# Performance work log

Measured on AMD Instinct MI355X. Metric: run time of the kernel, lower is better.

Reference implementation:

```python
import jax, jax.numpy as jnp
import numpy as np

D_MODEL = 1024
H = 16
D_H = D_MODEL // H
B = 8
S = 1024
NEG_INF = -1e9


def setup_inputs() -> dict:
    key = jax.random.key(0)
    ks = jax.random.split(key, 8)
    Qs = jax.random.normal(ks[0], (B, S, D_MODEL), dtype=jnp.float32)
    Ks = jax.random.normal(ks[1], (B, S, D_MODEL), dtype=jnp.float32)
    Vs = jax.random.normal(ks[2], (B, S, D_MODEL), dtype=jnp.float32)
    mask_3d = jnp.zeros((B, S, S), dtype=bool)
    # Parameters: torch.rand -> uniform[0,1) for per-head projections
    W_Q = jax.random.uniform(ks[3], (H, D_MODEL, D_H), dtype=jnp.float32)
    W_K = jax.random.uniform(ks[4], (H, D_MODEL, D_H), dtype=jnp.float32)
    W_V = jax.random.uniform(ks[5], (H, D_MODEL, D_H), dtype=jnp.float32)
    # Output nn.Linear(h*d_h, d_model): weight [d_model, h*d_h], bias [d_model]
    lim = 1.0 / np.sqrt(H * D_H)
    W_out = jax.random.uniform(ks[6], (D_MODEL, H * D_H), minval=-lim, maxval=lim, dtype=jnp.float32)
    b_out = jax.random.uniform(ks[7], (D_MODEL,), minval=-lim, maxval=lim, dtype=jnp.float32)
    return {"Qs": Qs, "Ks": Ks, "Vs": Vs, "mask_3d": mask_3d,
            "W_Q": W_Q, "W_K": W_K, "W_V": W_V, "W_out": W_out, "b_out": b_out}


def reference(Qs, Ks, Vs, mask_3d, W_Q, W_K, W_V, W_out, b_out):
    # Fused per-head projections: avoid the explicit repeat in the torch code.
    q = jnp.einsum('bsk,hkl->bhsl', Qs, W_Q)  # [B,H,S,D_H]
    k = jnp.einsum('bsk,hkl->bhsl', Ks, W_K)
    v = jnp.einsum('bsk,hkl->bhsl', Vs, W_V)
    scale = 1.0 / jnp.sqrt(jnp.asarray(D_H, dtype=q.dtype))
    scores = jnp.einsum('bhqd,bhkd->bhqk', q, k) * scale  # [B,H,S,S]
    scores = jnp.where(mask_3d[:, None, :, :], NEG_INF, scores)
    attn = jax.nn.softmax(scores, axis=-1)
    out = jnp.einsum('bhqk,bhkd->bhqd', attn, v)  # [B,H,S,D_H]
    # chunk along head-batch dim then cat along feature dim == head-major concat
    out = jnp.transpose(out, (0, 2, 1, 3)).reshape(B, S, H * D_H)
    return out @ W_out.T + b_out
```

## Files before the change

kernel.cpp:

```cpp
#include <hip/hip_runtime.h>

#define DM 1024
#define H_ 16
#define DH 64
#define B_ 8
#define S_ 1024

typedef _Float16 half8 __attribute__((ext_vector_type(8)));
typedef _Float16 half4 __attribute__((ext_vector_type(4)));
typedef float f32x4 __attribute__((ext_vector_type(4)));
typedef float f32x16 __attribute__((ext_vector_type(16)));
typedef unsigned int uint;

static __device__ inline uint pkh(float a, float b) {
    _Float16 ha = (_Float16)a, hb = (_Float16)b;
    unsigned short ua = __builtin_bit_cast(unsigned short, ha);
    unsigned short ub = __builtin_bit_cast(unsigned short, hb);
    return (uint)ua | ((uint)ub << 16);
}
#define PSWAP(d, s) asm volatile("v_permlane32_swap_b32 %0, %1" : "+v"(d), "+v"(s))

static __device__ __forceinline__ void gload16(const _Float16* g, _Float16* l) {
    __builtin_amdgcn_global_load_lds(
        (const __attribute__((address_space(1))) unsigned int*)(const void*)g,
        (__attribute__((address_space(3))) unsigned int*)(void*)l,
        16, 0, 0);
}

__global__ __launch_bounds__(256) void packw_k(
    const float* __restrict__ WQ, const float* __restrict__ WK,
    const float* __restrict__ WV,
    _Float16* __restrict__ wqh, _Float16* __restrict__ wql,
    _Float16* __restrict__ wkh, _Float16* __restrict__ wkl,
    _Float16* __restrict__ wv)
{
    __shared__ __align__(16) _Float16 Lh[64][72];
    __shared__ __align__(16) _Float16 Ll[64][72];
    const int t = threadIdx.x;
    const int kb = blockIdx.x;
    const int h  = blockIdx.y;

    #pragma unroll
    for (int s = 0; s < 3; ++s) {
        const float* W = (s == 0) ? WQ : ((s == 1) ? WK : WV);
        const int krow = t >> 2, lc = t & 3;
        const float* rp = W + (((size_t)h * 1024 + kb * 64 + krow) * 64 + lc * 16);
        #pragma unroll
        for (int q4 = 0; q4 < 4; ++q4) {
            float4 f = ((const float4*)rp)[q4];
            float vv0 = f.x, vv1 = f.y, vv2 = f.z, vv3 = f.w;
            int l0 = lc * 16 + q4 * 4;
            _Float16 h0 = (_Float16)vv0; Lh[l0 + 0][krow] = h0; Ll[l0 + 0][krow] = (_Float16)(vv0 - (float)h0);
            _Float16 h1 = (_Float16)vv1; Lh[l0 + 1][krow] = h1; Ll[l0 + 1][krow] = (_Float16)(vv1 - (float)h1);
            _Float16 h2 = (_Float16)vv2; Lh[l0 + 2][krow] = h2; Ll[l0 + 2][krow] = (_Float16)(vv2 - (float)h2);
            _Float16 h3 = (_Float16)vv3; Lh[l0 + 3][krow] = h3; Ll[l0 + 3][krow] = (_Float16)(vv3 - (float)h3);
        }
        __syncthreads();
        const int l = t >> 2, pc = t & 3;
        #pragma unroll
        for (int hp = 0; hp < 2; ++hp) {
            int p = pc + 4 * hp;
            int lc2 = p ^ (l & 7);
            half8 vh = *(const half8*)&Lh[l][lc2 * 8];
            half8 vl = *(const half8*)&Ll[l][lc2 * 8];
            size_t off = (size_t)(h * 64 + l) * DM + kb * 64 + p * 8;
            if (s == 0) { *(half8*)(wqh + off) = vh; *(half8*)(wql + off) = vl; }
            else if (s == 1) { *(half8*)(wkh + off) = vh; *(half8*)(wkl + off) = vl; }
            else { *(half8*)(wv + off) = vh; }
        }
        __syncthreads();
    }
}

__global__ __launch_bounds__(256) void packo_k(
    const float* __restrict__ WO, _Float16* __restrict__ wo)
{
    int idx8 = blockIdx.x * 256 + threadIdx.x;
    int n = idx8 >> 7;
    int c = idx8 & 127;
    int p = (c & ~7) | ((c & 7) ^ (n & 7));
    const float* rp = WO + ((size_t)n * DM + c * 8);
    float4 a = ((const float4*)rp)[0];
    float4 b = ((const float4*)rp)[1];
    half8 v;
    v[0] = (_Float16)a.x; v[1] = (_Float16)a.y; v[2] = (_Float16)a.z; v[3] = (_Float16)a.w;
    v[4] = (_Float16)b.x; v[5] = (_Float16)b.y; v[6] = (_Float16)b.z; v[7] = (_Float16)b.w;
    *(half8*)(wo + (size_t)n * DM + p * 8) = v;
}

__global__ __launch_bounds__(256) void scan_k(
    const unsigned char* __restrict__ mask, unsigned char* __restrict__ scan)
{
    __shared__ int s_red[4];
    const int t = threadIdx.x;
    const int q64 = blockIdx.x, k64 = blockIdx.y, b = blockIdx.z;
    uint4 mv = *(const uint4*)(mask + ((size_t)b * S_ + q64 * 64 + (t >> 2)) * S_ + k64 * 64 + (t & 3) * 16);
    int a = (mv.x | mv.y | mv.z | mv.w) != 0;
    unsigned long long bal = __ballot(a);
    if ((t & 63) == 0) s_red[t >> 6] = (bal != 0ull);
    __syncthreads();
    if (t == 0)
        scan[(b * 16 + q64) * 16 + k64] =
            (unsigned char)(s_red[0] | s_red[1] | s_red[2] | s_red[3]);
}

__global__ __launch_bounds__(256) void gemm_split_k(
    const float* __restrict__ A0, const float* __restrict__ A1,
    const _Float16* __restrict__ Bh0, const _Float16* __restrict__ Bl0,
    const _Float16* __restrict__ Bh1, const _Float16* __restrict__ Bl1,
    _Float16* __restrict__ Chi0, _Float16* __restrict__ Clo0,
    _Float16* __restrict__ Chi1, _Float16* __restrict__ Clo1)
{
    const int lid = blockIdx.x + 8 * blockIdx.y + 512 * blockIdx.z;
    const int xcd = lid & 7, k2 = lid >> 3;
    const int G = xcd * 16 + (k2 >> 3);
    const int bxv = k2 & 7, byv = G & 63, z = G >> 6;

    const float* A = z ? A1 : A0;
    const _Float16* Bh = z ? Bh1 : Bh0;
    const _Float16* Bl = z ? Bl1 : Bl0;
    _Float16* Chi = z ? Chi1 : Chi0;
    _Float16* Clo = z ? Clo1 : Clo0;

    __shared__ __align__(16) _Float16 SM[34816];
    _Float16* Ah  = SM;
    _Float16* Al  = SM + 9216;
    _Float16* Bhs = SM + 18432;
    _Float16* Bls = SM + 26624;

    const int t = threadIdx.x;
    const int lane = t & 63;
    const int w = t >> 6;
    const int wm = (w >> 1) * 64;
    const int wn = (w & 1) * 64;
    const int l15 = lane & 15;
    const int l4g = lane >> 4;

    const int bm = byv * 128;
    const int bn = bxv * 128;

    f32x4 acc[4][4] = {};

    const int arow = t >> 4, ac4 = t & 15;
    float4 ar[8];
    auto aload = [&](int KT) {
        #pragma unroll
        for (int i = 0; i < 8; ++i)
            ar[i] = *(const float4*)(A + (size_t)(bm + arow + 16 * i) * DM + KT * 64 + ac4 * 4);
    };
    auto awr = [&]() {
        #pragma unroll
        for (int i = 0; i < 8; ++i) {
            float4 v = ar[i];
            half4 hv, lv;
            hv[0] = (_Float16)v.x; lv[0] = (_Float16)(v.x - (float)hv[0]);
            hv[1] = (_Float16)v.y; lv[1] = (_Float16)(v.y - (float)hv[1]);
            hv[2] = (_Float16)v.z; lv[2] = (_Float16)(v.z - (float)hv[2]);
            hv[3] = (_Float16)v.w; lv[3] = (_Float16)(v.w - (float)hv[3]);
            *(half4*)&Ah[(arow + 16 * i) * 72 + ac4 * 4] = hv;
            *(half4*)&Al[(arow + 16 * i) * 72 + ac4 * 4] = lv;
        }
    };
    auto bgl = [&](int KT) {
        #pragma unroll
        for (int j = 0; j < 4; ++j) {
            int rr = w * 32 + j * 8 + (lane >> 3);
            const size_t so = (size_t)(bn + rr) * DM + KT * 64 + (lane & 7) * 8;
            gload16(Bh + so, &Bhs[(w * 32 + j * 8) * 64]);
            gload16(Bl + so, &Bls[(w * 32 + j * 8) * 64]);
        }
    };

    aload(0);
    bgl(0);
    for (int kt = 0; kt < 16; ++kt) {
        awr();
        __syncthreads();
        if (kt < 15) aload(kt + 1);
        #pragma unroll
        for (int ks = 0; ks < 2; ++ks) {
            half8 ah[4], al[4], bh[4], bl[4];
            #pragma unroll
            for (int mi = 0; mi < 4; ++mi) {
                ah[mi] = *(const half8*)&Ah[(wm + mi * 16 + l15) * 72 + ks * 32 + l4g * 8];
                al[mi] = *(const half8*)&Al[(wm + mi * 16 + l15) * 72 + ks * 32 + l4g * 8];
            }
            #pragma unroll
            for (int ni = 0; ni < 4; ++ni) {
                int row = wn + ni * 16 + l15;
                int slot = (ks * 4 + l4g) ^ (l15 & 7);
                bh[ni] = *(const half8*)&Bhs[row * 64 + slot * 8];
                bl[ni] = *(const half8*)&Bls[row * 64 + slot * 8];
            }
            #pragma unroll
            for (int mi = 0; mi < 4; ++mi)
                #pragma unroll
                for (int ni = 0; ni < 4; ++ni) {
                    acc[mi][ni] = __builtin_amdgcn_mfma_f32_16x16x32_f16(ah[mi], bh[ni], acc[mi][ni], 0, 0, 0);
                    acc[mi][ni] = __builtin_amdgcn_mfma_f32_16x16x32_f16(ah[mi], bl[ni], acc[mi][ni], 0, 0, 0);
                    acc[mi][ni] = __builtin_amdgcn_mfma_f32_16x16x32_f16(al[mi], bh[ni], acc[mi][ni], 0, 0, 0);
                }
        }
        __syncthreads();
        if (kt < 15) bgl(kt + 1);
    }

    #pragma unroll
    for (int mi = 0; mi < 4; ++mi)
        #pragma unroll
        for (int ni = 0; ni < 4; ++ni) {
            int col = bn + wn + ni * 16 + l15;
            #pragma unroll
            for (int r = 0; r < 4; ++r) {
                int row = bm + wm + mi * 16 + l4g * 4 + r;
                float val = acc[mi][ni][r];
                _Float16 hv = (_Float16)val;
                Chi[(size_t)row * DM + col] = hv;
                Clo[(size_t)row * DM + col] = (_Float16)(val - (float)hv);
            }
        }
}

__global__ __launch_bounds__(256) void gemm_v_k(
    const float* __restrict__ A, const _Float16* __restrict__ Bt,
    _Float16* __restrict__ C)
{
    const int lid = blockIdx.x + 8 * blockIdx.y;
    const int xcd = lid & 7, k2 = lid >> 3;
    const int G = xcd * 8 + (k2 >> 3);
    const int bxv = k2 & 7, byv = G;

    __shared__ __align__(16) _Float16 SM[25600];
    _Float16* As  = SM;
    _Float16* Bsb = SM + 9216;

    const int t = threadIdx.x;
    const int lane = t & 63;
    const int w = t >> 6;
    const int wm = (w >> 1) * 64;
    const int wn = (w & 1) * 64;
    const int l15 = lane & 15;
    const int l4g = lane >> 4;

    const int bm = byv * 128;
    const int bn = bxv * 128;

    f32x4 acc[4][4] = {};

    const int arow = t >> 4, ac4 = t & 15;
    float4 ar[8];
    auto aload = [&](int KT) {
        #pragma unroll
        for (int i = 0; i < 8; ++i)
            ar[i] = *(const float4*)(A + (size_t)(bm + arow + 16 * i) * DM + KT * 64 + ac4 * 4);
    };
    auto awr = [&]() {
        #pragma unroll
        for (int i = 0; i < 8; ++i) {
            float4 v = ar[i];
            half4 hv;
            hv[0] = (_Float16)v.x; hv[1] = (_Float16)v.y;
            hv[2] = (_Float16)v.z; hv[3] = (_Float16)v.w;
            *(half4*)&As[(arow + 16 * i) * 72 + ac4 * 4] = hv;
        }
    };
    auto bgl = [&](int KT, int buf) {
        _Float16* Bd = Bsb + buf * 8192;
        #pragma unroll
        for (int j = 0; j < 4; ++j) {
            int rr = w * 32 + j * 8 + (lane >> 3);
            gload16(Bt + (size_t)(bn + rr) * DM + KT * 64 + (lane & 7) * 8,
                    &Bd[(w * 32 + j * 8) * 64]);
        }
    };

    aload(0);
    bgl(0, 0);
    for (int kt = 0; kt < 16; ++kt) {
        const _Float16* Bcur = Bsb + (kt & 1) * 8192;
        awr();
        __syncthreads();
        if (kt < 15) { aload(kt + 1); bgl(kt + 1, (kt + 1) & 1); }
        #pragma unroll
        for (int ks = 0; ks < 2; ++ks) {
            half8 a[4], b[4];
            #pragma unroll
            for (int mi = 0; mi < 4; ++mi)
                a[mi] = *(const half8*)&As[(wm + mi * 16 + l15) * 72 + ks * 32 + l4g * 8];
            #pragma unroll
            for (int ni = 0; ni < 4; ++ni) {
                int row = wn + ni * 16 + l15;
                int slot = (ks * 4 + l4g) ^ (l15 & 7);
                b[ni] = *(const half8*)&Bcur[row * 64 + slot * 8];
            }
            #pragma unroll
            for (int mi = 0; mi < 4; ++mi)
                #pragma unroll
                for (int ni = 0; ni < 4; ++ni)
                    acc[mi][ni] = __builtin_amdgcn_mfma_f32_16x16x32_f16(a[mi], b[ni], acc[mi][ni], 0, 0, 0);
        }
        __syncthreads();
    }

    _Float16* Tw = SM + w * 4608;
    #pragma unroll
    for (int mi = 0; mi < 4; ++mi)
        #pragma unroll
        for (int ni = 0; ni < 4; ++ni)
            #pragma unroll
            for (int r = 0; r < 4; ++r)
                Tw[(ni * 16 + l15) * 72 + mi * 16 + l4g * 4 + r] = (_Float16)acc[mi][ni][r];
    __syncthreads();
    {
        const int mg0 = bm + wm;
        const int b = mg0 >> 10, s0 = mg0 & 1023;
        _Float16* op = C + ((size_t)b * DM + (bn + wn + lane)) * S_ + s0;
        #pragma unroll
        for (int c8 = 0; c8 < 8; ++c8)
            *(half8*)(op + c8 * 8) = *(const half8*)&Tw[lane * 72 + c8 * 8];
    }
}

__global__ __launch_bounds__(256) void gemm_out_k(
    const _Float16* __restrict__ A, const _Float16* __restrict__ Bt,
    float* __restrict__ C, const float* __restrict__ bias)
{
    const int lid = blockIdx.x + 8 * blockIdx.y;
    const int xcd = lid & 7, k2 = lid >> 3;
    const int G = xcd * 8 + (k2 >> 3);
    const int bxv = k2 & 7, byv = G;

    __shared__ __align__(16) _Float16 SM[25600];
    _Float16* As  = SM;
    _Float16* Bsb = SM + 9216;

    const int t = threadIdx.x;
    const int lane = t & 63;
    const int w = t >> 6;
    const int wm = (w >> 1) * 64;
    const int wn = (w & 1) * 64;
    const int l15 = lane & 15;
    const int l4g = lane >> 4;

    const int bm = byv * 128;
    const int bn = bxv * 128;

    f32x4 acc[4][4] = {};

    uint4 arr[4];
    auto aload = [&](int KT) {
        #pragma unroll
        for (int i = 0; i < 4; ++i)
            arr[i] = *(const uint4*)(A + (size_t)(bm + (t >> 3) + 32 * i) * DM + KT * 64 + (t & 7) * 8);
    };
    auto awr = [&]() {
        #pragma unroll
        for (int i = 0; i < 4; ++i)
            *(uint4*)&As[((t >> 3) + 32 * i) * 72 + (t & 7) * 8] = arr[i];
    };
    auto bgl = [&](int KT, int buf) {
        _Float16* Bd = Bsb + buf * 8192;
        #pragma unroll
        for (int j = 0; j < 4; ++j) {
            int rr = w * 32 + j * 8 + (lane >> 3);
            gload16(Bt + (size_t)(bn + rr) * DM + KT * 64 + (lane & 7) * 8,
                    &Bd[(w * 32 + j * 8) * 64]);
        }
    };

    aload(0);
    bgl(0, 0);
    for (int kt = 0; kt < 16; ++kt) {
        const _Float16* Bcur = Bsb + (kt & 1) * 8192;
        awr();
        __syncthreads();
        if (kt < 15) { aload(kt + 1); bgl(kt + 1, (kt + 1) & 1); }
        #pragma unroll
        for (int ks = 0; ks < 2; ++ks) {
            half8 a[4], b[4];
            #pragma unroll
            for (int mi = 0; mi < 4; ++mi)
                a[mi] = *(const half8*)&As[(wm + mi * 16 + l15) * 72 + ks * 32 + l4g * 8];
            #pragma unroll
            for (int ni = 0; ni < 4; ++ni) {
                int row = wn + ni * 16 + l15;
                int slot = (ks * 4 + l4g) ^ (l15 & 7);
                b[ni] = *(const half8*)&Bcur[row * 64 + slot * 8];
            }
            #pragma unroll
            for (int mi = 0; mi < 4; ++mi)
                #pragma unroll
                for (int ni = 0; ni < 4; ++ni)
                    acc[mi][ni] = __builtin_amdgcn_mfma_f32_16x16x32_f16(a[mi], b[ni], acc[mi][ni], 0, 0, 0);
        }
        __syncthreads();
    }

    #pragma unroll
    for (int mi = 0; mi < 4; ++mi)
        #pragma unroll
        for (int ni = 0; ni < 4; ++ni) {
            int col = bn + wn + ni * 16 + l15;
            #pragma unroll
            for (int r = 0; r < 4; ++r) {
                int row = bm + wm + mi * 16 + l4g * 4 + r;
                C[(size_t)row * DM + col] = acc[mi][ni][r] + bias[col];
            }
        }
}

__global__ __launch_bounds__(256) void attn_k(
    const _Float16* __restrict__ qhg, const _Float16* __restrict__ qlg,
    const _Float16* __restrict__ khg, const _Float16* __restrict__ klg,
    const _Float16* __restrict__ vtg, const unsigned char* __restrict__ maskg,
    const unsigned char* __restrict__ scanp, _Float16* __restrict__ ho)
{
    __shared__ __align__(16) _Float16 Kh[64][72];
    __shared__ __align__(16) _Float16 Kl[64][72];
    __shared__ __align__(16) _Float16 Vt[64][72];

    const int t = threadIdx.x;
    const int lane = t & 63;
    const int w = t >> 6;
    const int l31 = lane & 31;
    const int hi = lane >> 5;

    const int j = blockIdx.y + 16 * blockIdx.z;
    const int head = 16 * blockIdx.x + (j >> 3);
    const int qt = j & 7;
    const int h = head & 15;
    const int b = head >> 4;

    const int colbase = h * DH;
    const int qrow = qt * 128 + w * 32 + l31;

    half8 qfh[4], qfl[4];
    {
        const size_t base = ((size_t)b * S_ + qrow) * DM + colbase;
        #pragma unroll
        for (int ds = 0; ds < 4; ++ds) {
            qfh[ds] = *(const half8*)(qhg + base + ds * 16 + hi * 8);
            qfl[ds] = *(const half8*)(qlg + base + ds * 16 + hi * 8);
        }
    }

    float m_q = -1e30f, ls = 0.0f;
    f32x16 accO0 = {};
    f32x16 accO1 = {};

    const int r0 = t >> 3;
    const int c0 = (t & 7) * 8;
    const _Float16* kph = khg + ((size_t)b * S_) * DM + colbase;
    const _Float16* kpl = klg + ((size_t)b * S_) * DM + colbase;
    const _Float16* vp  = vtg + ((size_t)b * DM + colbase) * S_;
    const unsigned char* sc0 = scanp + (b * 16 + 2 * qt) * 16;
    const unsigned char* sc1 = scanp + (b * 16 + 2 * qt + 1) * 16;

    uint4 akh0, akh1, akl0, akl1, av0, av1;
#define ALOAD(KT) do { \
        akh0 = *(const uint4*)(kph + (size_t)((KT) * 64 + r0) * DM + c0);       \
        akh1 = *(const uint4*)(kph + (size_t)((KT) * 64 + 32 + r0) * DM + c0);  \
        akl0 = *(const uint4*)(kpl + (size_t)((KT) * 64 + r0) * DM + c0);       \
        akl1 = *(const uint4*)(kpl + (size_t)((KT) * 64 + 32 + r0) * DM + c0);  \
        av0  = *(const uint4*)(vp + (size_t)r0 * S_ + (KT) * 64 + c0);          \
        av1  = *(const uint4*)(vp + (size_t)(32 + r0) * S_ + (KT) * 64 + c0);   \
    } while (0)
#define AWRITE() do { \
        *(uint4*)&Kh[r0][c0] = akh0; *(uint4*)&Kh[32 + r0][c0] = akh1; \
        *(uint4*)&Kl[r0][c0] = akl0; *(uint4*)&Kl[32 + r0][c0] = akl1; \
        *(uint4*)&Vt[r0][c0] = av0;  *(uint4*)&Vt[32 + r0][c0] = av1;  \
    } while (0)

    ALOAD(0);
    AWRITE();
    int msk = sc0[0] | sc1[0];

    const float SC = 0.125f * 1.44269504089f;

    for (int kt = 0; kt < 16; ++kt) {
        __syncthreads();
        const int mskcur = msk;
        if (kt < 15) {
            ALOAD(kt + 1);
            msk = sc0[kt + 1] | sc1[kt + 1];
        }

        f32x16 sa0 = {}, sa1 = {};
        #pragma unroll
        for (int ds = 0; ds < 4; ++ds) {
            half8 kh0 = *(const half8*)&Kh[l31][ds * 16 + hi * 8];
            half8 kl0 = *(const half8*)&Kl[l31][ds * 16 + hi * 8];
            half8 kh1 = *(const half8*)&Kh[32 + l31][ds * 16 + hi * 8];
            half8 kl1 = *(const half8*)&Kl[32 + l31][ds * 16 + hi * 8];
            sa0 = __builtin_amdgcn_mfma_f32_32x32x16_f16(kh0, qfh[ds], sa0, 0, 0, 0);
            sa0 = __builtin_amdgcn_mfma_f32_32x32x16_f16(kh0, qfl[ds], sa0, 0, 0, 0);
            sa0 = __builtin_amdgcn_mfma_f32_32x32x16_f16(kl0, qfh[ds], sa0, 0, 0, 0);
            sa1 = __builtin_amdgcn_mfma_f32_32x32x16_f16(kh1, qfh[ds], sa1, 0, 0, 0);
            sa1 = __builtin_amdgcn_mfma_f32_32x32x16_f16(kh1, qfl[ds], sa1, 0, 0, 0);
            sa1 = __builtin_amdgcn_mfma_f32_32x32x16_f16(kl1, qfh[ds], sa1, 0, 0, 0);
        }
        #pragma unroll
        for (int e = 0; e < 16; ++e) { sa0[e] *= SC; sa1[e] *= SC; }

        if (mskcur) {
            const unsigned char* mrow = maskg + ((size_t)b * S_ + qrow) * S_ + kt * 64;
            #pragma unroll
            for (int e = 0; e < 16; ++e) {
                int kl_ = (e & 3) + 8 * (e >> 2) + 4 * hi;
                if (mrow[kl_]) sa0[e] = -1e9f;
                if (mrow[32 + kl_]) sa1[e] = -1e9f;
            }
        }

        float rm = sa0[0];
        #pragma unroll
        for (int e = 1; e < 16; ++e) rm = fmaxf(rm, sa0[e]);
        #pragma unroll
        for (int e = 0; e < 16; ++e) rm = fmaxf(rm, sa1[e]);
        rm = fmaxf(rm, __shfl_xor(rm, 32));
        const float mn = fmaxf(m_q, rm);
        const float sfac = exp2f(m_q - mn);
        m_q = mn;
        float rs = 0.0f;
        #pragma unroll
        for (int e = 0; e < 16; ++e) { sa0[e] = exp2f(sa0[e] - mn); rs += sa0[e]; }
        #pragma unroll
        for (int e = 0; e < 16; ++e) { sa1[e] = exp2f(sa1[e] - mn); rs += sa1[e]; }
        rs += __shfl_xor(rs, 32);
        ls = ls * sfac + rs;
        #pragma unroll
        for (int e = 0; e < 16; ++e) { accO0[e] *= sfac; accO1[e] *= sfac; }

        half8 pf[4];
        {
            uint c0_ = pkh(sa0[0], sa0[1]),  c1_ = pkh(sa0[2], sa0[3]);
            uint c2_ = pkh(sa0[4], sa0[5]),  c3_ = pkh(sa0[6], sa0[7]);
            uint c4_ = pkh(sa0[8], sa0[9]),  c5_ = pkh(sa0[10], sa0[11]);
            uint c6_ = pkh(sa0[12], sa0[13]), c7_ = pkh(sa0[14], sa0[15]);
            PSWAP(c0_, c2_); PSWAP(c1_, c3_);
            PSWAP(c4_, c6_); PSWAP(c5_, c7_);
            uint4 u0 = {c0_, c1_, c2_, c3_}, u1 = {c4_, c5_, c6_, c7_};
            pf[0] = __builtin_bit_cast(half8, u0);
            pf[1] = __builtin_bit_cast(half8, u1);
        }
        {
            uint c0_ = pkh(sa1[0], sa1[1]),  c1_ = pkh(sa1[2], sa1[3]);
            uint c2_ = pkh(sa1[4], sa1[5]),  c3_ = pkh(sa1[6], sa1[7]);
            uint c4_ = pkh(sa1[8], sa1[9]),  c5_ = pkh(sa1[10], sa1[11]);
            uint c6_ = pkh(sa1[12], sa1[13]), c7_ = pkh(sa1[14], sa1[15]);
            PSWAP(c0_, c2_); PSWAP(c1_, c3_);
            PSWAP(c4_, c6_); PSWAP(c5_, c7_);
            uint4 u0 = {c0_, c1_, c2_, c3_}, u1 = {c4_, c5_, c6_, c7_};
            pf[2] = __builtin_bit_cast(half8, u0);
            pf[3] = __builtin_bit_cast(half8, u1);
        }
        #pragma unroll
        for (int kc = 0; kc < 4; ++kc) {
            half8 vf0 = *(const half8*)&Vt[l31][kc * 16 + hi * 8];
            half8 vf1 = *(const half8*)&Vt[32 + l31][kc * 16 + hi * 8];
            accO0 = __builtin_amdgcn_mfma_f32_32x32x16_f16(vf0, pf[kc], accO0, 0, 0, 0);
            accO1 = __builtin_amdgcn_mfma_f32_32x32x16_f16(vf1, pf[kc], accO1, 0, 0, 0);
        }

        __syncthreads();
        if (kt < 15) AWRITE();
    }
#undef ALOAD
#undef AWRITE

    const float inv = 1.0f / ls;
    _Float16* orow = ho + ((size_t)b * S_ + qrow) * DM + colbase;
    #pragma unroll
    for (int g2 = 0; g2 < 4; ++g2) {
        half4 hv0, hv1;
        #pragma unroll
        for (int e = 0; e < 4; ++e) {
            hv0[e] = (_Float16)(accO0[g2 * 4 + e] * inv);
            hv1[e] = (_Float16)(accO1[g2 * 4 + e] * inv);
        }
        *(half4*)(orow + g2 * 8 + hi * 4) = hv0;
        *(half4*)(orow + 32 + g2 * 8 + hi * 4) = hv1;
    }
}

extern "C" void kernel_launch(void* const* d_in, const int* in_sizes, int n_in,
                              void* d_out, int out_size, void* d_ws, size_t ws_size,
                              hipStream_t stream)
{
    const float* Qs = (const float*)d_in[0];
    const float* Ks = (const float*)d_in[1];
    const float* Vs = (const float*)d_in[2];
    const unsigned char* mask = (const unsigned char*)d_in[3];
    const float* WQ = (const float*)d_in[4];
    const float* WK = (const float*)d_in[5];
    const float* WV = (const float*)d_in[6];
    const float* WO = (const float*)d_in[7];
    const float* bo = (const float*)d_in[8];

    char* ws = (char*)d_ws;
    const size_t MB = 1024 * 1024;
    _Float16* wqh = (_Float16*)(ws + 0 * MB);
    _Float16* wql = (_Float16*)(ws + 2 * MB);
    _Float16* wkh = (_Float16*)(ws + 4 * MB);
    _Float16* wkl = (_Float16*)(ws + 6 * MB);
    _Float16* wv  = (_Float16*)(ws + 8 * MB);
    _Float16* wo  = (_Float16*)(ws + 10 * MB);
    _Float16* qhi = (_Float16*)(ws + 12 * MB);
    _Float16* qlo = (_Float16*)(ws + 28 * MB);
    _Float16* khi = (_Float16*)(ws + 44 * MB);
    _Float16* klo = (_Float16*)(ws + 60 * MB);
    _Float16* vt  = (_Float16*)(ws + 76 * MB);
    _Float16* hh  = (_Float16*)(ws + 92 * MB);
    unsigned char* scan = (unsigned char*)(ws + 108 * MB);

    packw_k<<<dim3(16, 16), 256, 0, stream>>>(WQ, WK, WV, wqh, wql, wkh, wkl, wv);
    packo_k<<<512, 256, 0, stream>>>(WO, wo);
    scan_k<<<dim3(16, 16, 8), 256, 0, stream>>>(mask, scan);

    gemm_split_k<<<dim3(8, 64, 2), 256, 0, stream>>>(
        Qs, Ks, wqh, wql, wkh, wkl, qhi, qlo, khi, klo);

    gemm_v_k<<<dim3(8, 64), 256, 0, stream>>>(Vs, wv, vt);

    attn_k<<<dim3(8, 16, 8), 256, 0, stream>>>(qhi, qlo, khi, klo, vt, mask, scan, hh);

    gemm_out_k<<<dim3(8, 64), 256, 0, stream>>>(hh, wo, (float*)d_out, bo);
}
```

Before: 310.1 us.

## Use 512-thread split GEMM, lazy softmax rescale, pkrtz packing and MFMA priority

The split-precision Q/K projection GEMM moves to 512 threads per block with 32-row warp tiles and an XOR-swizzled unpadded A tile in LDS, halving per-thread accumulators and loads. In the attention kernel the per-element score scaling is folded into an FMA inside exp2, and the running max and output rescale are only updated when some lane's row max exceeds the old max by a threshold. Probability packing switches to the hardware round-toward-zero pack instruction, and MFMA blocks are wrapped in s_setprio raises. These target register pressure, LDS padding and VALU work in the softmax, at the cost of slightly different rounding and a threshold-based lazy rescale that allows exp values to grow before renormalising.

```diff
diff --git a/kernel.cpp b/kernel.cpp
--- a/kernel.cpp
+++ b/kernel.cpp
@@ -8,15 +8,14 @@
 
 typedef _Float16 half8 __attribute__((ext_vector_type(8)));
 typedef _Float16 half4 __attribute__((ext_vector_type(4)));
+typedef __fp16 fp16x2 __attribute__((ext_vector_type(2)));
 typedef float f32x4 __attribute__((ext_vector_type(4)));
 typedef float f32x16 __attribute__((ext_vector_type(16)));
 typedef unsigned int uint;
 
-static __device__ inline uint pkh(float a, float b) {
-    _Float16 ha = (_Float16)a, hb = (_Float16)b;
-    unsigned short ua = __builtin_bit_cast(unsigned short, ha);
-    unsigned short ub = __builtin_bit_cast(unsigned short, hb);
-    return (uint)ua | ((uint)ub << 16);
+static __device__ __forceinline__ uint pkrtz(float a, float b) {
+    fp16x2 h = __builtin_amdgcn_cvt_pkrtz(a, b);
+    return __builtin_bit_cast(uint, h);
 }
 #define PSWAP(d, s) asm volatile("v_permlane32_swap_b32 %0, %1" : "+v"(d), "+v"(s))
 
@@ -104,7 +103,7 @@
             (unsigned char)(s_red[0] | s_red[1] | s_red[2] | s_red[3]);
 }
 
-__global__ __launch_bounds__(256) void gemm_split_k(
+__global__ __launch_bounds__(512) void gemm_split_k(
     const float* __restrict__ A0, const float* __restrict__ A1,
     const _Float16* __restrict__ Bh0, const _Float16* __restrict__ Bl0,
     const _Float16* __restrict__ Bh1, const _Float16* __restrict__ Bl1,
@@ -122,16 +121,16 @@
     _Float16* Chi = z ? Chi1 : Chi0;
     _Float16* Clo = z ? Clo1 : Clo0;
 
-    __shared__ __align__(16) _Float16 SM[34816];
+    __shared__ __align__(16) _Float16 SM[32768];
     _Float16* Ah  = SM;
-    _Float16* Al  = SM + 9216;
-    _Float16* Bhs = SM + 18432;
-    _Float16* Bls = SM + 26624;
+    _Float16* Al  = SM + 8192;
+    _Float16* Bhs = SM + 16384;
+    _Float16* Bls = SM + 24576;
 
     const int t = threadIdx.x;
     const int lane = t & 63;
     const int w = t >> 6;
-    const int wm = (w >> 1) * 64;
+    const int wm = (w >> 1) * 32;
     const int wn = (w & 1) * 64;
     const int l15 = lane & 15;
     const int l4g = lane >> 4;
@@ -139,35 +138,37 @@
     const int bm = byv * 128;
     const int bn = bxv * 128;
 
-    f32x4 acc[4][4] = {};
-
-    const int arow = t >> 4, ac4 = t & 15;
-    float4 ar[8];
+    f32x4 acc[2][4] = {};
+
+    float4 ar[4];
     auto aload = [&](int KT) {
         #pragma unroll
-        for (int i = 0; i < 8; ++i)
-            ar[i] = *(const float4*)(A + (size_t)(bm + arow + 16 * i) * DM + KT * 64 + ac4 * 4);
+        for (int i = 0; i < 4; ++i)
+            ar[i] = *(const float4*)(A + (size_t)(bm + (t >> 4) + 32 * i) * DM + KT * 64 + (t & 15) * 4);
     };
     auto awr = [&]() {
         #pragma unroll
-        for (int i = 0; i < 8; ++i) {
+        for (int i = 0; i < 4; ++i) {
+            int row = (t >> 4) + 32 * i;
+            int c4 = t & 15;
             float4 v = ar[i];
             half4 hv, lv;
             hv[0] = (_Float16)v.x; lv[0] = (_Float16)(v.x - (float)hv[0]);
             hv[1] = (_Float16)v.y; lv[1] = (_Float16)(v.y - (float)hv[1]);
             hv[2] = (_Float16)v.z; lv[2] = (_Float16)(v.z - (float)hv[2]);
             hv[3] = (_Float16)v.w; lv[3] = (_Float16)(v.w - (float)hv[3]);
-            *(half4*)&Ah[(arow + 16 * i) * 72 + ac4 * 4] = hv;
-            *(half4*)&Al[(arow + 16 * i) * 72 + ac4 * 4] = lv;
+            int off = row * 64 + (((c4 >> 1) ^ (row & 7)) * 8) + (c4 & 1) * 4;
+            *(half4*)&Ah[off] = hv;
+            *(half4*)&Al[off] = lv;
         }
     };
     auto bgl = [&](int KT) {
         #pragma unroll
-        for (int j = 0; j < 4; ++j) {
-            int rr = w * 32 + j * 8 + (lane >> 3);
+        for (int j = 0; j < 2; ++j) {
+            int rr = w * 16 + j * 8 + (lane >> 3);
             const size_t so = (size_t)(bn + rr) * DM + KT * 64 + (lane & 7) * 8;
-            gload16(Bh + so, &Bhs[(w * 32 + j * 8) * 64]);
-            gload16(Bl + so, &Bls[(w * 32 + j * 8) * 64]);
+            gload16(Bh + so, &Bhs[(w * 16 + j * 8) * 64]);
+            gload16(Bl + so, &Bls[(w * 16 + j * 8) * 64]);
         }
     };
 
@@ -179,21 +180,24 @@
         if (kt < 15) aload(kt + 1);
         #pragma unroll
         for (int ks = 0; ks < 2; ++ks) {
-            half8 ah[4], al[4], bh[4], bl[4];
-            #pragma unroll
-            for (int mi = 0; mi < 4; ++mi) {
-                ah[mi] = *(const half8*)&Ah[(wm + mi * 16 + l15) * 72 + ks * 32 + l4g * 8];
-                al[mi] = *(const half8*)&Al[(wm + mi * 16 + l15) * 72 + ks * 32 + l4g * 8];
+            half8 ah[2], al[2], bh[4], bl[4];
+            const int slotx = (ks * 4 + l4g);
+            #pragma unroll
+            for (int mi = 0; mi < 2; ++mi) {
+                int r = wm + mi * 16 + l15;
+                int off = r * 64 + (slotx ^ (l15 & 7)) * 8;
+                ah[mi] = *(const half8*)&Ah[off];
+                al[mi] = *(const half8*)&Al[off];
             }
             #pragma unroll
             for (int ni = 0; ni < 4; ++ni) {
-                int row = wn + ni * 16 + l15;
-                int slot = (ks * 4 + l4g) ^ (l15 & 7);
-                bh[ni] = *(const half8*)&Bhs[row * 64 + slot * 8];
-                bl[ni] = *(const half8*)&Bls[row * 64 + slot * 8];
+                int r = wn + ni * 16 + l15;
+                int off = r * 64 + (slotx ^ (l15 & 7)) * 8;
+                bh[ni] = *(const half8*)&Bhs[off];
+                bl[ni] = *(const half8*)&Bls[off];
             }
             #pragma unroll
-            for (int mi = 0; mi < 4; ++mi)
+            for (int mi = 0; mi < 2; ++mi)
                 #pragma unroll
                 for (int ni = 0; ni < 4; ++ni) {
                     acc[mi][ni] = __builtin_amdgcn_mfma_f32_16x16x32_f16(ah[mi], bh[ni], acc[mi][ni], 0, 0, 0);
@@ -206,7 +210,7 @@
     }
 
     #pragma unroll
-    for (int mi = 0; mi < 4; ++mi)
+    for (int mi = 0; mi < 2; ++mi)
         #pragma unroll
         for (int ni = 0; ni < 4; ++ni) {
             int col = bn + wn + ni * 16 + l15;
@@ -476,6 +480,7 @@
     int msk = sc0[0] | sc1[0];
 
     const float SC = 0.125f * 1.44269504089f;
+    const float THRRAW = 8.0f / SC;
 
     for (int kt = 0; kt < 16; ++kt) {
         __syncthreads();
@@ -486,6 +491,7 @@
         }
 
         f32x16 sa0 = {}, sa1 = {};
+        __builtin_amdgcn_s_setprio(1);
         #pragma unroll
         for (int ds = 0; ds < 4; ++ds) {
             half8 kh0 = *(const half8*)&Kh[l31][ds * 16 + hi * 8];
@@ -499,8 +505,7 @@
             sa1 = __builtin_amdgcn_mfma_f32_32x32x16_f16(kh1, qfl[ds], sa1, 0, 0, 0);
             sa1 = __builtin_amdgcn_mfma_f32_32x32x16_f16(kl1, qfh[ds], sa1, 0, 0, 0);
         }
-        #pragma unroll
-        for (int e = 0; e < 16; ++e) { sa0[e] *= SC; sa1[e] *= SC; }
+        __builtin_amdgcn_s_setprio(0);
 
         if (mskcur) {
             const unsigned char* mrow = maskg + ((size_t)b * S_ + qrow) * S_ + kt * 64;
@@ -518,25 +523,29 @@
         #pragma unroll
         for (int e = 0; e < 16; ++e) rm = fmaxf(rm, sa1[e]);
         rm = fmaxf(rm, __shfl_xor(rm, 32));
-        const float mn = fmaxf(m_q, rm);
-        const float sfac = exp2f(m_q - mn);
-        m_q = mn;
+        if (__any(rm > m_q + THRRAW)) {
+            const float mn = fmaxf(m_q, rm);
+            const float sfac = exp2f((m_q - mn) * SC);
+            m_q = mn;
+            ls *= sfac;
+            #pragma unroll
+            for (int e = 0; e < 16; ++e) { accO0[e] *= sfac; accO1[e] *= sfac; }
+        }
+        const float nmn = -m_q * SC;
         float rs = 0.0f;
         #pragma unroll
-        for (int e = 0; e < 16; ++e) { sa0[e] = exp2f(sa0[e] - mn); rs += sa0[e]; }
-        #pragma unroll
-        for (int e = 0; e < 16; ++e) { sa1[e] = exp2f(sa1[e] - mn); rs += sa1[e]; }
+        for (int e = 0; e < 16; ++e) { sa0[e] = exp2f(fmaf(sa0[e], SC, nmn)); rs += sa0[e]; }
+        #pragma unroll
+        for (int e = 0; e < 16; ++e) { sa1[e] = exp2f(fmaf(sa1[e], SC, nmn)); rs += sa1[e]; }
         rs += __shfl_xor(rs, 32);
-        ls = ls * sfac + rs;
-        #pragma unroll
-        for (int e = 0; e < 16; ++e) { accO0[e] *= sfac; accO1[e] *= sfac; }
+        ls += rs;
 
         half8 pf[4];
         {
-            uint c0_ = pkh(sa0[0], sa0[1]),  c1_ = pkh(sa0[2], sa0[3]);
-            uint c2_ = pkh(sa0[4], sa0[5]),  c3_ = pkh(sa0[6], sa0[7]);
-            uint c4_ = pkh(sa0[8], sa0[9]),  c5_ = pkh(sa0[10], sa0[11]);
-            uint c6_ = pkh(sa0[12], sa0[13]), c7_ = pkh(sa0[14], sa0[15]);
+            uint c0_ = pkrtz(sa0[0], sa0[1]),  c1_ = pkrtz(sa0[2], sa0[3]);
+            uint c2_ = pkrtz(sa0[4], sa0[5]),  c3_ = pkrtz(sa0[6], sa0[7]);
+            uint c4_ = pkrtz(sa0[8], sa0[9]),  c5_ = pkrtz(sa0[10], sa0[11]);
+            uint c6_ = pkrtz(sa0[12], sa0[13]), c7_ = pkrtz(sa0[14], sa0[15]);
             PSWAP(c0_, c2_); PSWAP(c1_, c3_);
             PSWAP(c4_, c6_); PSWAP(c5_, c7_);
             uint4 u0 = {c0_, c1_, c2_, c3_}, u1 = {c4_, c5_, c6_, c7_};
@@ -544,16 +553,17 @@
             pf[1] = __builtin_bit_cast(half8, u1);
         }
         {
-            uint c0_ = pkh(sa1[0], sa1[1]),  c1_ = pkh(sa1[2], sa1[3]);
-            uint c2_ = pkh(sa1[4], sa1[5]),  c3_ = pkh(sa1[6], sa1[7]);
-            uint c4_ = pkh(sa1[8], sa1[9]),  c5_ = pkh(sa1[10], sa1[11]);
-            uint c6_ = pkh(sa1[12], sa1[13]), c7_ = pkh(sa1[14], sa1[15]);
+            uint c0_ = pkrtz(sa1[0], sa1[1]),  c1_ = pkrtz(sa1[2], sa1[3]);
+            uint c2_ = pkrtz(sa1[4], sa1[5]),  c3_ = pkrtz(sa1[6], sa1[7]);
+            uint c4_ = pkrtz(sa1[8], sa1[9]),  c5_ = pkrtz(sa1[10], sa1[11]);
+            uint c6_ = pkrtz(sa1[12], sa1[13]), c7_ = pkrtz(sa1[14], sa1[15]);
             PSWAP(c0_, c2_); PSWAP(c1_, c3_);
             PSWAP(c4_, c6_); PSWAP(c5_, c7_);
             uint4 u0 = {c0_, c1_, c2_, c3_}, u1 = {c4_, c5_, c6_, c7_};
             pf[2] = __builtin_bit_cast(half8, u0);
             pf[3] = __builtin_bit_cast(half8, u1);
         }
+        __builtin_amdgcn_s_setprio(1);
         #pragma unroll
         for (int kc = 0; kc < 4; ++kc) {
             half8 vf0 = *(const half8*)&Vt[l31][kc * 16 + hi * 8];
@@ -561,6 +571,7 @@
             accO0 = __builtin_amdgcn_mfma_f32_32x32x16_f16(vf0, pf[kc], accO0, 0, 0, 0);
             accO1 = __builtin_amdgcn_mfma_f32_32x32x16_f16(vf1, pf[kc], accO1, 0, 0, 0);
         }
+        __builtin_amdgcn_s_setprio(0);
 
         __syncthreads();
         if (kt < 15) AWRITE();
@@ -617,7 +628,7 @@
     packo_k<<<512, 256, 0, stream>>>(WO, wo);
     scan_k<<<dim3(16, 16, 8), 256, 0, stream>>>(mask, scan);
 
-    gemm_split_k<<<dim3(8, 64, 2), 256, 0, stream>>>(
+    gemm_split_k<<<dim3(8, 64, 2), 512, 0, stream>>>(
         Qs, Ks, wqh, wql, wkh, wkl, qhi, qlo, khi, klo);
 
     gemm_v_k<<<dim3(8, 64), 256, 0, stream>>>(Vs, wv, vt);
```

Result: no change. 305.7 us (-1.4%).
